# Kernel tuning notes

Measured on AMD Instinct MI355X. Metric: run time of the kernel, lower is better.

The kernel has to match this reference:

```python
import jax, jax.numpy as jnp
import numpy as np

N, D, E, DFF = 8192, 1024, 8, 4096


def setup_inputs() -> dict:
    key = jax.random.key(0)
    k1, k2, k3, k4 = jax.random.split(key, 4)
    x = jax.random.normal(k1, (N, D), dtype=jnp.float32)
    gate_w = jax.random.normal(k2, (D, E), dtype=jnp.float32) * 0.02
    w1 = jax.random.normal(k3, (E, D, DFF), dtype=jnp.float32) * 0.02
    w2 = jax.random.normal(k4, (E, DFF, D), dtype=jnp.float32) * 0.02
    return {"x": x, "gate_w": gate_w, "w1": w1, "w2": w2, "top_k": 2}


def reference(x, gate_w, w1, w2, top_k):
    # Router: softmax over experts, top-k, renormalize top-k weights.
    gate_logits = x @ gate_w                          # [N, E]
    gate_probs = jax.nn.softmax(gate_logits, axis=-1)  # [N, E]
    top_w, top_i = jax.lax.top_k(gate_probs, top_k)    # [N, k]
    top_w = top_w / jnp.sum(top_w, axis=-1, keepdims=True)
    # Dense combine weights: zero except at the top-k experts per token.
    n = x.shape[0]
    dense_w = jnp.zeros_like(gate_probs).at[jnp.arange(n)[:, None], top_i].set(top_w)  # [N, E]
    # Per-expert SiLU MLP, weighted combine. Loop over small fixed E.
    y = jnp.zeros_like(x)
    for e in range(w1.shape[0]):
        h = jax.nn.silu(x @ w1[e]) @ w2[e]            # [N, D]
        y = y + dense_w[:, e:e + 1] * h
    return y
```

## Files before the change

### kernel.cpp

```cpp
#include <hip/hip_runtime.h>


#define N_TOK 8192
#define DIM   1024
#define NE    8
#define DFF   4096
#define BM 128
#define BN 128
#define BK 64
#define QE 4
#define KS2 4

typedef unsigned short u16;
typedef short bf16x8 __attribute__((ext_vector_type(8)));
typedef float f32x4  __attribute__((ext_vector_type(4)));

#define TOKE_OFF   0u
#define TOKW_OFF   32768u
#define TLIST_OFF  65536u
#define WLIST_OFF  131072u
#define COUNTS_OFF 196608u
#define BASEP_OFF  196672u
#define CURSOR_OFF 196736u
#define XB_OFF     1048576u
#define H_OFF      17825792u
#define WT_OFF     152043520u

__device__ __forceinline__ float bf2f(u16 h) {
    return __uint_as_float(((unsigned)h) << 16);
}
__device__ __forceinline__ u16 f2bf(float f) {
    unsigned u = __float_as_uint(f);
    unsigned r = u + 0x7FFFu + ((u >> 16) & 1u);
    return (u16)(r >> 16);
}

#define GLL16(g, l)                                                             \
    __builtin_amdgcn_global_load_lds(                                           \
        (const __attribute__((address_space(1))) unsigned int*)(g),             \
        (__attribute__((address_space(3))) unsigned int*)(l), 16, 0, 0)

__global__ void convtrans(const float* __restrict__ in, u16* __restrict__ out,
                          int R, int C) {
    __shared__ float tile[32][33];
    int z = blockIdx.z;
    const float* src = in  + (size_t)z * R * C;
    u16*         dst = out + (size_t)z * R * C;
    int c0 = blockIdx.x * 32, r0 = blockIdx.y * 32;
    int tx = threadIdx.x & 31, ty = threadIdx.x >> 5;
#pragma unroll
    for (int i = 0; i < 32; i += 8)
        tile[ty + i][tx] = src[(size_t)(r0 + ty + i) * C + c0 + tx];
    __syncthreads();
#pragma unroll
    for (int i = 0; i < 32; i += 8)
        dst[(size_t)(c0 + ty + i) * R + r0 + tx] = f2bf(tile[tx][ty + i]);
}

__global__ __launch_bounds__(256) void gate_kernel(
        const float* __restrict__ x, const float* __restrict__ gw,
        u16* __restrict__ xb, int* __restrict__ tok_e, float* __restrict__ tok_w,
        int* __restrict__ counts) {
    __shared__ float gsm[NE * DIM];
    __shared__ int hcnt[NE];
    int tid = threadIdx.x;
    if (tid < NE) hcnt[tid] = 0;
    for (int i = tid; i < NE * DIM; i += 256) {
        int d = i >> 3, e = i & 7;
        gsm[e * DIM + d] = gw[i];
    }
    __syncthreads();
    int lane = tid & 63, wid = tid >> 6;
    int t0 = blockIdx.x * 32 + wid * 8;
    for (int tt = 0; tt < 8; ++tt) {
        int t = t0 + tt;
        const float4* xr  = (const float4*)(x  + (size_t)t * DIM);
        ushort4*      xbr = (ushort4*)(xb + (size_t)t * DIM);
        float acc[NE];
#pragma unroll
        for (int e = 0; e < NE; ++e) acc[e] = 0.f;
#pragma unroll
        for (int j = 0; j < 4; ++j) {
            float4 xv = xr[j * 64 + lane];
            ushort4 o;
            o.x = f2bf(xv.x); o.y = f2bf(xv.y); o.z = f2bf(xv.z); o.w = f2bf(xv.w);
            xbr[j * 64 + lane] = o;
            int dbase = (j * 64 + lane) * 4;
#pragma unroll
            for (int e = 0; e < NE; ++e) {
                float4 g = *(const float4*)&gsm[e * DIM + dbase];
                acc[e] += xv.x * g.x + xv.y * g.y + xv.z * g.z + xv.w * g.w;
            }
        }
#pragma unroll
        for (int off = 32; off > 0; off >>= 1) {
#pragma unroll
            for (int e = 0; e < NE; ++e) acc[e] += __shfl_xor(acc[e], off, 64);
        }
        if (lane == 0) {
            int a = 0;
#pragma unroll
            for (int e = 1; e < NE; ++e) if (acc[e] > acc[a]) a = e;
            int b = (a == 0) ? 1 : 0;
#pragma unroll
            for (int e = 0; e < NE; ++e) if (e != a && acc[e] > acc[b]) b = e;
            float wa = 1.f / (1.f + __expf(acc[b] - acc[a]));
            tok_e[t] = (a << 3) | b;
            tok_w[t] = wa;
            atomicAdd(&hcnt[a], 1);
            atomicAdd(&hcnt[b], 1);
        }
    }
    __syncthreads();
    if (tid < NE) atomicAdd(&counts[tid], hcnt[tid]);
}

__global__ void scan_kernel(const int* __restrict__ counts, int* __restrict__ basep,
                            int* __restrict__ cursor) {
    if (threadIdx.x == 0) {
        int s = 0;
        for (int e = 0; e < NE; ++e) { basep[e] = s; s += counts[e]; cursor[e] = 0; }
    }
}

__global__ void assign_kernel(const int* __restrict__ tok_e, const float* __restrict__ tok_w,
                              const int* __restrict__ basep, int* __restrict__ cursor,
                              int* __restrict__ tlist, float* __restrict__ wlist) {
    int t = blockIdx.x * 256 + threadIdx.x;
    if (t >= N_TOK) return;
    int ee = tok_e[t];
    int a = ee >> 3, b = ee & 7;
    float wa = tok_w[t];
    int pa = atomicAdd(&cursor[a], 1);
    int sa = basep[a] + pa;
    tlist[sa] = t;  wlist[sa] = wa;
    int pb = atomicAdd(&cursor[b], 1);
    int sb = basep[b] + pb;
    tlist[sb] = t;  wlist[sb] = 1.f - wa;
}

__global__ __launch_bounds__(256) void gemm1_silu(
        const u16* __restrict__ xb, const u16* __restrict__ w1t,
        const int* __restrict__ tlist, const int* __restrict__ counts,
        const int* __restrict__ basep, u16* __restrict__ H, int ebase) {
    int bx = blockIdx.x;
    int le = bx >> 11;
    int e  = ebase + le;
    int mt = (bx >> 5) & 63;
    int nt = bx & 31;
    int cnt = counts[e];
    int row0 = mt * BM;
    if (row0 >= cnt) return;
    int nv = cnt - row0; if (nv > BM) nv = BM;
    int gb = basep[e] + row0;

    __shared__ __align__(16) u16 As[BM * BK];
    __shared__ __align__(16) u16 Bs[BN * BK];

    int tid = threadIdx.x;
    int lane = tid & 63, wid = tid >> 6;
    int wm = (wid & 1) * 64, wn = (wid >> 1) * 64;

    const u16* ga[4]; const u16* gbp[4]; int loff[4];
#pragma unroll
    for (int i = 0; i < 4; ++i) {
        int cidx = (wid * 4 + i) * 64 + lane;
        int row = cidx >> 3;
        int cg  = (cidx & 7) ^ (row & 7);
        int ra  = (row < nv) ? row : 0;
        ga[i]  = xb + (size_t)tlist[gb + ra] * DIM + cg * 8;
        gbp[i] = w1t + ((size_t)le * DFF + (size_t)nt * BN + row) * DIM + cg * 8;
        loff[i] = (wid * 4 + i) * 512;
    }

    f32x4 acc[4][4];
#pragma unroll
    for (int i = 0; i < 4; ++i)
#pragma unroll
        for (int j = 0; j < 4; ++j) acc[i][j] = (f32x4){0.f, 0.f, 0.f, 0.f};

    for (int k0 = 0; k0 < DIM; k0 += BK) {
#pragma unroll
        for (int i = 0; i < 4; ++i) {
            GLL16(ga[i] + k0, &As[loff[i]]);
            GLL16(gbp[i] + k0, &Bs[loff[i]]);
        }
        __syncthreads();
#pragma unroll
        for (int ks = 0; ks < 2; ++ks) {
            int kc = ks * 4 + (lane >> 4);
            bf16x8 af[4], bfr[4];
#pragma unroll
            for (int mi = 0; mi < 4; ++mi) {
                int r = wm + mi * 16 + (lane & 15);
                af[mi] = *(const bf16x8*)&As[(r * 8 + (kc ^ (r & 7))) * 8];
            }
#pragma unroll
            for (int ni = 0; ni < 4; ++ni) {
                int r = wn + ni * 16 + (lane & 15);
                bfr[ni] = *(const bf16x8*)&Bs[(r * 8 + (kc ^ (r & 7))) * 8];
            }
#pragma unroll
            for (int mi = 0; mi < 4; ++mi)
#pragma unroll
                for (int ni = 0; ni < 4; ++ni)
                    acc[mi][ni] = __builtin_amdgcn_mfma_f32_16x16x32_bf16(
                        af[mi], bfr[ni], acc[mi][ni], 0, 0, 0);
        }
        __syncthreads();
    }
#pragma unroll
    for (int mi = 0; mi < 4; ++mi) {
#pragma unroll
        for (int r = 0; r < 4; ++r) {
            int row = wm + mi * 16 + (lane >> 4) * 4 + r;
            if (row < nv) {
                size_t ho = (size_t)(gb + row) * DFF + nt * BN + wn + (lane & 15);
#pragma unroll
                for (int ni = 0; ni < 4; ++ni) {
                    float v = acc[mi][ni][r];
                    H[ho + ni * 16] = f2bf(v / (1.f + __expf(-v)));
                }
            }
        }
    }
}

__global__ __launch_bounds__(256) void gemm2_combine(
        const u16* __restrict__ H, const u16* __restrict__ w2t,
        const int* __restrict__ tlist, const float* __restrict__ wlist,
        const int* __restrict__ counts, const int* __restrict__ basep,
        float* __restrict__ y, int ebase) {
    int bx = blockIdx.x;
    int ksp = bx & (KS2 - 1);
    int nt  = (bx >> 2) & 7;
    int mt  = (bx >> 5) & 63;
    int le  = bx >> 11;
    int e   = ebase + le;
    int cnt = counts[e];
    int row0 = mt * BM;
    if (row0 >= cnt) return;
    int nv = cnt - row0; if (nv > BM) nv = BM;
    int gb = basep[e] + row0;

    __shared__ __align__(16) u16 As[BM * BK];
    __shared__ __align__(16) u16 Bs[BN * BK];

    int tid = threadIdx.x;
    int lane = tid & 63, wid = tid >> 6;
    int wm = (wid & 1) * 64, wn = (wid >> 1) * 64;

    const u16* ga[4]; const u16* gbp[4]; int loff[4];
#pragma unroll
    for (int i = 0; i < 4; ++i) {
        int cidx = (wid * 4 + i) * 64 + lane;
        int row = cidx >> 3;
        int cg  = (cidx & 7) ^ (row & 7);
        int ra  = (row < nv) ? row : 0;
        ga[i]  = H + (size_t)(gb + ra) * DFF + cg * 8;
        gbp[i] = w2t + ((size_t)le * DIM + (size_t)nt * BN + row) * DFF + cg * 8;
        loff[i] = (wid * 4 + i) * 512;
    }

    f32x4 acc[4][4];
#pragma unroll
    for (int i = 0; i < 4; ++i)
#pragma unroll
        for (int j = 0; j < 4; ++j) acc[i][j] = (f32x4){0.f, 0.f, 0.f, 0.f};

    int kbeg = ksp * (DFF / KS2);
    for (int k0 = kbeg; k0 < kbeg + DFF / KS2; k0 += BK) {
#pragma unroll
        for (int i = 0; i < 4; ++i) {
            GLL16(ga[i] + k0, &As[loff[i]]);
            GLL16(gbp[i] + k0, &Bs[loff[i]]);
        }
        __syncthreads();
#pragma unroll
        for (int ks = 0; ks < 2; ++ks) {
            int kc = ks * 4 + (lane >> 4);
            bf16x8 af[4], bfr[4];
#pragma unroll
            for (int mi = 0; mi < 4; ++mi) {
                int r = wm + mi * 16 + (lane & 15);
                af[mi] = *(const bf16x8*)&As[(r * 8 + (kc ^ (r & 7))) * 8];
            }
#pragma unroll
            for (int ni = 0; ni < 4; ++ni) {
                int r = wn + ni * 16 + (lane & 15);
                bfr[ni] = *(const bf16x8*)&Bs[(r * 8 + (kc ^ (r & 7))) * 8];
            }
#pragma unroll
            for (int mi = 0; mi < 4; ++mi)
#pragma unroll
                for (int ni = 0; ni < 4; ++ni)
                    acc[mi][ni] = __builtin_amdgcn_mfma_f32_16x16x32_bf16(
                        af[mi], bfr[ni], acc[mi][ni], 0, 0, 0);
        }
        __syncthreads();
    }
#pragma unroll
    for (int mi = 0; mi < 4; ++mi) {
#pragma unroll
        for (int r = 0; r < 4; ++r) {
            int row = wm + mi * 16 + (lane >> 4) * 4 + r;
            if (row < nv) {
                int gslot = gb + row;
                int t = tlist[gslot];
                float w = wlist[gslot];
                size_t yo = (size_t)t * DIM + nt * BN + wn + (lane & 15);
#pragma unroll
                for (int ni = 0; ni < 4; ++ni)
                    atomicAdd(&y[yo + ni * 16], w * acc[mi][ni][r]);
            }
        }
    }
}

extern "C" void kernel_launch(void* const* d_in, const int* in_sizes, int n_in,
                              void* d_out, int out_size, void* d_ws, size_t ws_size,
                              hipStream_t stream) {
    const float* x  = (const float*)d_in[0];
    const float* gw = (const float*)d_in[1];
    const float* w1 = (const float*)d_in[2];
    const float* w2 = (const float*)d_in[3];
    float* y = (float*)d_out;

    char* ws = (char*)d_ws;
    int*   tok_e  = (int*)(ws + TOKE_OFF);
    float* tok_w  = (float*)(ws + TOKW_OFF);
    int*   tlist  = (int*)(ws + TLIST_OFF);
    float* wlist  = (float*)(ws + WLIST_OFF);
    int*   counts = (int*)(ws + COUNTS_OFF);
    int*   basep  = (int*)(ws + BASEP_OFF);
    int*   cursor = (int*)(ws + CURSOR_OFF);
    u16*   xb     = (u16*)(ws + XB_OFF);
    u16*   H      = (u16*)(ws + H_OFF);
    u16*   wt     = (u16*)(ws + WT_OFF);

    hipMemsetAsync(counts, 0, 32, stream);
    hipMemsetAsync(y, 0, (size_t)N_TOK * DIM * sizeof(float), stream);
    gate_kernel<<<N_TOK / 32, 256, 0, stream>>>(x, gw, xb, tok_e, tok_w, counts);
    scan_kernel<<<1, 64, 0, stream>>>(counts, basep, cursor);
    assign_kernel<<<N_TOK / 256, 256, 0, stream>>>(tok_e, tok_w, basep, cursor, tlist, wlist);
    for (int q = 0; q < NE / QE; ++q) {
        convtrans<<<dim3(DFF / 32, DIM / 32, QE), 256, 0, stream>>>(
            w1 + (size_t)q * QE * DIM * DFF, wt, DIM, DFF);
        gemm1_silu<<<QE * 64 * 32, 256, 0, stream>>>(xb, wt, tlist, counts, basep, H, q * QE);
    }
    for (int q = 0; q < NE / QE; ++q) {
        convtrans<<<dim3(DIM / 32, DFF / 32, QE), 256, 0, stream>>>(
            w2 + (size_t)q * QE * DFF * DIM, wt, DFF, DIM);
        gemm2_combine<<<QE * 64 * 8 * KS2, 256, 0, stream>>>(H, wt, tlist, wlist, counts,
                                                             basep, y, q * QE);
    }
}
```

Baseline: 1.012 ms.

## Double-buffer gemm2 LDS loads, halve split-K, and vectorize weight transpose

The gemm2_combine kernel now uses two LDS buffers so the next K tile's global-to-LDS loads overlap the current tile's MFMA work, synchronised with explicit vmcnt waits and barriers. Split-K drops from 4 to 2, which halves the fp32 atomicAdd traffic into y but gives fewer blocks and longer per-block K loops. The block index decode is reordered to match. The weight convert-transpose kernel now reads float4 and writes ushort4 per thread, replacing scalar accesses to cut memory transactions. The doubled LDS footprint may lower occupancy.

Result: faster. 952.8 us (-5.9%).

```diff
diff --git a/kernel.cpp b/kernel.cpp
--- a/kernel.cpp
+++ b/kernel.cpp
@@ -9,7 +9,8 @@
 #define BN 128
 #define BK 64
 #define QE 4
-#define KS2 4
+#define KS2 2
+#define NT2 (DFF / KS2 / BK)
 
 typedef unsigned short u16;
 typedef short bf16x8 __attribute__((ext_vector_type(8)));
@@ -40,21 +41,22 @@
         (const __attribute__((address_space(1))) unsigned int*)(g),             \
         (__attribute__((address_space(3))) unsigned int*)(l), 16, 0, 0)
 
-__global__ void convtrans(const float* __restrict__ in, u16* __restrict__ out,
-                          int R, int C) {
-    __shared__ float tile[32][33];
+__global__ __launch_bounds__(256) void convtrans(
+        const float* __restrict__ in, u16* __restrict__ out, int R, int C) {
+    __shared__ float t[32][33];
     int z = blockIdx.z;
     const float* src = in  + (size_t)z * R * C;
     u16*         dst = out + (size_t)z * R * C;
     int c0 = blockIdx.x * 32, r0 = blockIdx.y * 32;
-    int tx = threadIdx.x & 31, ty = threadIdx.x >> 5;
-#pragma unroll
-    for (int i = 0; i < 32; i += 8)
-        tile[ty + i][tx] = src[(size_t)(r0 + ty + i) * C + c0 + tx];
+    int tx = threadIdx.x & 7, ty = threadIdx.x >> 3;
+    float4 v = *(const float4*)&src[(size_t)(r0 + ty) * C + c0 + tx * 4];
+    t[tx * 4 + 0][ty] = v.x;  t[tx * 4 + 1][ty] = v.y;
+    t[tx * 4 + 2][ty] = v.z;  t[tx * 4 + 3][ty] = v.w;
     __syncthreads();
-#pragma unroll
-    for (int i = 0; i < 32; i += 8)
-        dst[(size_t)(c0 + ty + i) * R + r0 + tx] = f2bf(tile[tx][ty + i]);
+    ushort4 o;
+    o.x = f2bf(t[ty][tx * 4 + 0]);  o.y = f2bf(t[ty][tx * 4 + 1]);
+    o.z = f2bf(t[ty][tx * 4 + 2]);  o.w = f2bf(t[ty][tx * 4 + 3]);
+    *(ushort4*)&dst[(size_t)(c0 + ty) * R + r0 + tx * 4] = o;
 }
 
 __global__ __launch_bounds__(256) void gate_kernel(
@@ -232,10 +234,10 @@
         const int* __restrict__ counts, const int* __restrict__ basep,
         float* __restrict__ y, int ebase) {
     int bx = blockIdx.x;
-    int ksp = bx & (KS2 - 1);
-    int nt  = (bx >> 2) & 7;
-    int mt  = (bx >> 5) & 63;
-    int le  = bx >> 11;
+    int le  = bx >> 10;
+    int mt  = (bx >> 4) & 63;
+    int nt  = (bx >> 1) & 7;
+    int ksp = bx & 1;
     int e   = ebase + le;
     int cnt = counts[e];
     int row0 = mt * BM;
@@ -243,8 +245,8 @@
     int nv = cnt - row0; if (nv > BM) nv = BM;
     int gb = basep[e] + row0;
 
-    __shared__ __align__(16) u16 As[BM * BK];
-    __shared__ __align__(16) u16 Bs[BN * BK];
+    __shared__ __align__(16) u16 As[2][BM * BK];
+    __shared__ __align__(16) u16 Bs[2][BN * BK];
 
     int tid = threadIdx.x;
     int lane = tid & 63, wid = tid >> 6;
@@ -268,37 +270,57 @@
 #pragma unroll
         for (int j = 0; j < 4; ++j) acc[i][j] = (f32x4){0.f, 0.f, 0.f, 0.f};
 
+#define STAGE2(buf, kk)                                                         \
+    do {                                                                        \
+        _Pragma("unroll")                                                       \
+        for (int i = 0; i < 4; ++i) {                                           \
+            GLL16(ga[i] + (kk), &As[buf][loff[i]]);                             \
+            GLL16(gbp[i] + (kk), &Bs[buf][loff[i]]);                            \
+        }                                                                       \
+    } while (0)
+
+#define COMPUTE2(buf)                                                           \
+    do {                                                                        \
+        _Pragma("unroll")                                                       \
+        for (int ks = 0; ks < 2; ++ks) {                                        \
+            int kc = ks * 4 + (lane >> 4);                                      \
+            bf16x8 af[4], bfr[4];                                               \
+            _Pragma("unroll")                                                   \
+            for (int mi = 0; mi < 4; ++mi) {                                    \
+                int r = wm + mi * 16 + (lane & 15);                             \
+                af[mi] = *(const bf16x8*)&As[buf][(r * 8 + (kc ^ (r & 7))) * 8];\
+            }                                                                   \
+            _Pragma("unroll")                                                   \
+            for (int ni = 0; ni < 4; ++ni) {                                    \
+                int r = wn + ni * 16 + (lane & 15);                             \
+                bfr[ni] = *(const bf16x8*)&Bs[buf][(r * 8 + (kc ^ (r & 7))) * 8];\
+            }                                                                   \
+            _Pragma("unroll")                                                   \
+            for (int mi = 0; mi < 4; ++mi)                                      \
+                _Pragma("unroll")                                               \
+                for (int ni = 0; ni < 4; ++ni)                                  \
+                    acc[mi][ni] = __builtin_amdgcn_mfma_f32_16x16x32_bf16(      \
+                        af[mi], bfr[ni], acc[mi][ni], 0, 0, 0);                 \
+        }                                                                       \
+    } while (0)
+
     int kbeg = ksp * (DFF / KS2);
-    for (int k0 = kbeg; k0 < kbeg + DFF / KS2; k0 += BK) {
-#pragma unroll
-        for (int i = 0; i < 4; ++i) {
-            GLL16(ga[i] + k0, &As[loff[i]]);
-            GLL16(gbp[i] + k0, &Bs[loff[i]]);
-        }
-        __syncthreads();
-#pragma unroll
-        for (int ks = 0; ks < 2; ++ks) {
-            int kc = ks * 4 + (lane >> 4);
-            bf16x8 af[4], bfr[4];
-#pragma unroll
-            for (int mi = 0; mi < 4; ++mi) {
-                int r = wm + mi * 16 + (lane & 15);
-                af[mi] = *(const bf16x8*)&As[(r * 8 + (kc ^ (r & 7))) * 8];
-            }
-#pragma unroll
-            for (int ni = 0; ni < 4; ++ni) {
-                int r = wn + ni * 16 + (lane & 15);
-                bfr[ni] = *(const bf16x8*)&Bs[(r * 8 + (kc ^ (r & 7))) * 8];
-            }
-#pragma unroll
-            for (int mi = 0; mi < 4; ++mi)
-#pragma unroll
-                for (int ni = 0; ni < 4; ++ni)
-                    acc[mi][ni] = __builtin_amdgcn_mfma_f32_16x16x32_bf16(
-                        af[mi], bfr[ni], acc[mi][ni], 0, 0, 0);
-        }
-        __syncthreads();
-    }
+    STAGE2(0, kbeg);
+    int cur = 0;
+    for (int t = 0; t < NT2 - 1; ++t) {
+        STAGE2(cur ^ 1, kbeg + (t + 1) * BK);
+        asm volatile("s_waitcnt vmcnt(8)" ::: "memory");
+        __builtin_amdgcn_s_barrier();
+        __builtin_amdgcn_sched_barrier(0);
+        COMPUTE2(cur);
+        __builtin_amdgcn_s_barrier();
+        cur ^= 1;
+    }
+    asm volatile("s_waitcnt vmcnt(0)" ::: "memory");
+    __builtin_amdgcn_s_barrier();
+    __builtin_amdgcn_sched_barrier(0);
+    COMPUTE2(cur);
+
 #pragma unroll
     for (int mi = 0; mi < 4; ++mi) {
 #pragma unroll
@@ -315,6 +337,8 @@
             }
         }
     }
+#undef STAGE2
+#undef COMPUTE2
 }
 
 extern "C" void kernel_launch(void* const* d_in, const int* in_sizes, int n_in,
```
